# Kernel tuning notes

Measured on AMD Instinct MI355X. Metric: run time of the kernel, lower is better.

## Reference

```python
import jax, jax.numpy as jnp
import numpy as np

CLAMP = 5.0

def setup_inputs() -> dict:
    key = jax.random.key(0)
    k1, k2, k3, k4, k5 = jax.random.split(key, 5)
    B, S, D, R = 4, 4096, 2048, 16
    v = jax.random.normal(k1, (B, S, D), dtype=jnp.float32)
    x = jax.random.normal(k2, (B, S, D), dtype=jnp.float32)
    # params; match torch init scale (0.001) for U/W; V is zero-init in the module,
    # but use small random so the modulation branch is exercised.
    U = jax.random.normal(k3, (D, R), dtype=jnp.float32) * 0.001
    W = jax.random.normal(k4, (D, R), dtype=jnp.float32) * 0.001
    Vw = jax.random.normal(k5, (1, D), dtype=jnp.float32) * 0.01
    return {"v": v, "x": x, "U": U, "W": W, "Vw": Vw}

def reference(v, x, U, W, Vw):
    # proj: [B,S,R] ; sq elementwise ; out: [B,S,D]
    proj = jnp.einsum('bsd,dr->bsr', v, U)
    sq = proj * proj
    out = jnp.einsum('bsr,dr->bsd', sq, W)
    # dynamic curvature modulation: sigmoid(V^T x), V is Linear(dim,1,no bias)
    modulation = jax.nn.sigmoid(jnp.einsum('bsd,od->bso', x, Vw))  # [B,S,1]
    out = out * (1.0 + modulation)
    return jnp.clip(out, -CLAMP, CLAMP)
```

## Files before the change

### kernel.cpp

```cpp
#include <hip/hip_runtime.h>
#include <math.h>


constexpr int D_DIM   = 2048;
constexpr int R_DIM   = 16;
constexpr int ROWS    = 64;
constexpr int THREADS = 1024;
constexpr int WAVES   = THREADS / 64;
constexpr int RB      = 2;

typedef float f32x2 __attribute__((ext_vector_type(2)));

constexpr int SMEM_FLOATS = R_DIM * D_DIM + D_DIM + ROWS * R_DIM + ROWS;
constexpr size_t SMEM_BYTES = (size_t)SMEM_FLOATS * sizeof(float);

__device__ __forceinline__ float clamp5(float v) {
    return fminf(fmaxf(v, -5.0f), 5.0f);
}
__device__ __forceinline__ float dot4(float4 a, float4 b) {
    return a.x * b.x + a.y * b.y + a.z * b.z + a.w * b.w;
}

extern "C" __global__ void __launch_bounds__(THREADS)
__attribute__((amdgpu_waves_per_eu(4, 4)))
lrc_kernel(const float* __restrict__ v, const float* __restrict__ x,
           const float* __restrict__ U, const float* __restrict__ W,
           const float* __restrict__ Vw, float* __restrict__ out, int nrows)
{
    extern __shared__ float smem[];
    float* u_lds   = smem;
    float* vw_lds  = u_lds + R_DIM * D_DIM;
    float* sq_lds  = vw_lds + D_DIM;
    float* fac_lds = sq_lds + ROWS * R_DIM;

    const int tid  = threadIdx.x;
    const int lane = tid & 63;
    const int wave = tid >> 6;
    const int row0 = blockIdx.x * ROWS;

    for (int i = tid; i < D_DIM / 4; i += THREADS)
        reinterpret_cast<float4*>(vw_lds)[i] = reinterpret_cast<const float4*>(Vw)[i];

    {
        const int dd = tid * 2;
        float u0[R_DIM], u1[R_DIM];
        const float4* p0 = reinterpret_cast<const float4*>(U + (size_t)dd * R_DIM);
        const float4* p1 = reinterpret_cast<const float4*>(U + (size_t)(dd + 1) * R_DIM);
        #pragma unroll
        for (int c = 0; c < 4; ++c) {
            *reinterpret_cast<float4*>(&u0[c * 4]) = p0[c];
            *reinterpret_cast<float4*>(&u1[c * 4]) = p1[c];
        }
        #pragma unroll
        for (int r = 0; r < R_DIM; ++r)
            *reinterpret_cast<float2*>(&u_lds[r * D_DIM + dd]) = make_float2(u0[r], u1[r]);
    }
    __syncthreads();

    #pragma unroll
    for (int b = 0; b < (ROWS / WAVES) / RB; ++b) {
        const int rl0 = wave * (ROWS / WAVES) + b * RB;
        const float* vb = v + (size_t)(row0 + rl0) * D_DIM;
        const float* xb = x + (size_t)(row0 + rl0) * D_DIM;

        float pp[RB][R_DIM];
        float xv[RB];
        #pragma unroll
        for (int k = 0; k < RB; ++k) {
            xv[k] = 0.0f;
            #pragma unroll
            for (int r = 0; r < R_DIM; ++r) pp[k][r] = 0.0f;
        }

        for (int i = 0; i < D_DIM / 256; ++i) {
            const int d0 = i * 256 + lane * 4;
            float4 v4[RB], x4[RB];
            #pragma unroll
            for (int k = 0; k < RB; ++k) {
                v4[k] = *reinterpret_cast<const float4*>(vb + (size_t)k * D_DIM + d0);
                x4[k] = *reinterpret_cast<const float4*>(xb + (size_t)k * D_DIM + d0);
            }
            const float4 vw4 = *reinterpret_cast<const float4*>(vw_lds + d0);
            #pragma unroll
            for (int k = 0; k < RB; ++k) xv[k] += dot4(x4[k], vw4);
            #pragma unroll
            for (int r = 0; r < R_DIM; ++r) {
                const float4 u4 = *reinterpret_cast<const float4*>(u_lds + r * D_DIM + d0);
                #pragma unroll
                for (int k = 0; k < RB; ++k) pp[k][r] += dot4(v4[k], u4);
            }
        }

        #pragma unroll
        for (int s = 32; s >= 1; s >>= 1) {
            #pragma unroll
            for (int k = 0; k < RB; ++k) {
                xv[k] += __shfl_xor(xv[k], s, 64);
                #pragma unroll
                for (int r = 0; r < R_DIM; ++r) pp[k][r] += __shfl_xor(pp[k][r], s, 64);
            }
        }
        if (lane == 0) {
            #pragma unroll
            for (int k = 0; k < RB; ++k) {
                const int rl = rl0 + k;
                if (row0 + rl < nrows) {
                    #pragma unroll
                    for (int r = 0; r < R_DIM; ++r)
                        sq_lds[rl * R_DIM + r] = pp[k][r] * pp[k][r];
                    fac_lds[rl] = 1.0f + 1.0f / (1.0f + __expf(-xv[k]));
                }
            }
        }
    }
    __syncthreads();

    {
        const int dd = tid * 2;
        float w0[R_DIM], w1[R_DIM];
        const float4* p0 = reinterpret_cast<const float4*>(W + (size_t)dd * R_DIM);
        const float4* p1 = reinterpret_cast<const float4*>(W + (size_t)(dd + 1) * R_DIM);
        #pragma unroll
        for (int c = 0; c < 4; ++c) {
            *reinterpret_cast<float4*>(&w0[c * 4]) = p0[c];
            *reinterpret_cast<float4*>(&w1[c * 4]) = p1[c];
        }

        for (int rl = 0; rl < ROWS; ++rl) {
            if (row0 + rl >= nrows) break;
            float sqv[R_DIM];
            #pragma unroll
            for (int c = 0; c < 4; ++c)
                *reinterpret_cast<float4*>(&sqv[c * 4]) =
                    *reinterpret_cast<const float4*>(sq_lds + rl * R_DIM + c * 4);
            const float fac = fac_lds[rl];
            float o0 = 0.0f, o1 = 0.0f;
            #pragma unroll
            for (int r = 0; r < R_DIM; ++r) {
                o0 += sqv[r] * w0[r];
                o1 += sqv[r] * w1[r];
            }
            f32x2 o;
            o.x = clamp5(o0 * fac);
            o.y = clamp5(o1 * fac);
            __builtin_nontemporal_store(o,
                reinterpret_cast<f32x2*>(out + (size_t)(row0 + rl) * D_DIM + dd));
        }
    }
}

extern "C" void kernel_launch(void* const* d_in, const int* in_sizes, int n_in,
                              void* d_out, int out_size, void* d_ws, size_t ws_size,
                              hipStream_t stream) {
    const float* v  = (const float*)d_in[0];
    const float* x  = (const float*)d_in[1];
    const float* U  = (const float*)d_in[2];
    const float* W  = (const float*)d_in[3];
    const float* Vw = (const float*)d_in[4];
    float* out = (float*)d_out;

    const int nrows = in_sizes[0] / D_DIM;
    const int grid  = (nrows + ROWS - 1) / ROWS;

    (void)hipFuncSetAttribute((const void*)lrc_kernel,
                              hipFuncAttributeMaxDynamicSharedMemorySize,
                              (int)SMEM_BYTES);
    lrc_kernel<<<grid, THREADS, SMEM_BYTES, stream>>>(v, x, U, W, Vw, out, nrows);
}
```

Before: 84.52 us.

## Pre-transpose U in separate kernel, read U/Vw from global instead of LDS

Adds a small kernel that transposes U into the workspace so the main kernel can read U and Vw directly from global memory (through the caches) rather than staging them in 128 KB of LDS per block. Rows per block are halved to 32, so each wave handles a single pair of rows, and the forced waves-per-EU attribute is removed. The aim is to drop the per-block LDS fill and its sync and to let more blocks fit per CU. In exchange it adds an extra kernel launch and puts the per-iteration U reads on the cache hierarchy instead of LDS.

```diff
diff --git a/kernel.cpp b/kernel.cpp
--- a/kernel.cpp
+++ b/kernel.cpp
@@ -4,15 +4,12 @@
 
 constexpr int D_DIM   = 2048;
 constexpr int R_DIM   = 16;
-constexpr int ROWS    = 64;
+constexpr int ROWS    = 32;
 constexpr int THREADS = 1024;
 constexpr int WAVES   = THREADS / 64;
 constexpr int RB      = 2;
 
 typedef float f32x2 __attribute__((ext_vector_type(2)));
-
-constexpr int SMEM_FLOATS = R_DIM * D_DIM + D_DIM + ROWS * R_DIM + ROWS;
-constexpr size_t SMEM_BYTES = (size_t)SMEM_FLOATS * sizeof(float);
 
 __device__ __forceinline__ float clamp5(float v) {
     return fminf(fmaxf(v, -5.0f), 5.0f);
@@ -21,45 +18,31 @@
     return a.x * b.x + a.y * b.y + a.z * b.z + a.w * b.w;
 }
 
+extern "C" __global__ void transpose_u(const float* __restrict__ U,
+                                       float* __restrict__ Ut) {
+    const int o = blockIdx.x * blockDim.x + threadIdx.x;
+    if (o < R_DIM * D_DIM) {
+        const int r = o >> 11;
+        const int d = o & (D_DIM - 1);
+        Ut[o] = U[(d << 4) + r];
+    }
+}
+
 extern "C" __global__ void __launch_bounds__(THREADS)
-__attribute__((amdgpu_waves_per_eu(4, 4)))
 lrc_kernel(const float* __restrict__ v, const float* __restrict__ x,
-           const float* __restrict__ U, const float* __restrict__ W,
+           const float* __restrict__ Ut, const float* __restrict__ W,
            const float* __restrict__ Vw, float* __restrict__ out, int nrows)
 {
-    extern __shared__ float smem[];
-    float* u_lds   = smem;
-    float* vw_lds  = u_lds + R_DIM * D_DIM;
-    float* sq_lds  = vw_lds + D_DIM;
-    float* fac_lds = sq_lds + ROWS * R_DIM;
+    __shared__ float sq_lds[ROWS * R_DIM];
+    __shared__ float fac_lds[ROWS];
 
     const int tid  = threadIdx.x;
     const int lane = tid & 63;
     const int wave = tid >> 6;
     const int row0 = blockIdx.x * ROWS;
 
-    for (int i = tid; i < D_DIM / 4; i += THREADS)
-        reinterpret_cast<float4*>(vw_lds)[i] = reinterpret_cast<const float4*>(Vw)[i];
-
     {
-        const int dd = tid * 2;
-        float u0[R_DIM], u1[R_DIM];
-        const float4* p0 = reinterpret_cast<const float4*>(U + (size_t)dd * R_DIM);
-        const float4* p1 = reinterpret_cast<const float4*>(U + (size_t)(dd + 1) * R_DIM);
-        #pragma unroll
-        for (int c = 0; c < 4; ++c) {
-            *reinterpret_cast<float4*>(&u0[c * 4]) = p0[c];
-            *reinterpret_cast<float4*>(&u1[c * 4]) = p1[c];
-        }
-        #pragma unroll
-        for (int r = 0; r < R_DIM; ++r)
-            *reinterpret_cast<float2*>(&u_lds[r * D_DIM + dd]) = make_float2(u0[r], u1[r]);
-    }
-    __syncthreads();
-
-    #pragma unroll
-    for (int b = 0; b < (ROWS / WAVES) / RB; ++b) {
-        const int rl0 = wave * (ROWS / WAVES) + b * RB;
+        const int rl0 = wave * RB;
         const float* vb = v + (size_t)(row0 + rl0) * D_DIM;
         const float* xb = x + (size_t)(row0 + rl0) * D_DIM;
 
@@ -80,12 +63,13 @@
                 v4[k] = *reinterpret_cast<const float4*>(vb + (size_t)k * D_DIM + d0);
                 x4[k] = *reinterpret_cast<const float4*>(xb + (size_t)k * D_DIM + d0);
             }
-            const float4 vw4 = *reinterpret_cast<const float4*>(vw_lds + d0);
+            const float4 vw4 = *reinterpret_cast<const float4*>(Vw + d0);
             #pragma unroll
             for (int k = 0; k < RB; ++k) xv[k] += dot4(x4[k], vw4);
             #pragma unroll
             for (int r = 0; r < R_DIM; ++r) {
-                const float4 u4 = *reinterpret_cast<const float4*>(u_lds + r * D_DIM + d0);
+                const float4 u4 =
+                    *reinterpret_cast<const float4*>(Ut + r * D_DIM + d0);
                 #pragma unroll
                 for (int k = 0; k < RB; ++k) pp[k][r] += dot4(v4[k], u4);
             }
@@ -158,12 +142,11 @@
     const float* W  = (const float*)d_in[3];
     const float* Vw = (const float*)d_in[4];
     float* out = (float*)d_out;
+    float* Ut  = (float*)d_ws;
 
     const int nrows = in_sizes[0] / D_DIM;
     const int grid  = (nrows + ROWS - 1) / ROWS;
 
-    (void)hipFuncSetAttribute((const void*)lrc_kernel,
-                              hipFuncAttributeMaxDynamicSharedMemorySize,
-                              (int)SMEM_BYTES);
-    lrc_kernel<<<grid, THREADS, SMEM_BYTES, stream>>>(v, x, U, W, Vw, out, nrows);
+    transpose_u<<<(R_DIM * D_DIM + 255) / 256, 256, 0, stream>>>(U, Ut);
+    lrc_kernel<<<grid, THREADS, 0, stream>>>(v, x, Ut, W, Vw, out, nrows);
 }
```

Result: slower. 145.7 us (+72.4%).

## Keep per-row projections in registers and compute output per wave with transposed W

Applied to the files above, without the earlier changes.

Each wave now owns 4 rows end-to-end: it computes the rank-16 projections and modulation, squares them in registers, then directly produces the output rows using a pre-transposed W read as float4 from global memory. This removes the LDS staging of squared projections and the block-wide barrier between the reduction and output phases, and widens stores to float4. It adds a small extra transpose kernel launch per call, drops the partial-tail handling for incomplete row groups, and raises register pressure with RB=4 plus 16 float4 W values.

```diff
diff --git a/kernel.cpp b/kernel.cpp
--- a/kernel.cpp
+++ b/kernel.cpp
@@ -6,12 +6,11 @@
 constexpr int R_DIM   = 16;
 constexpr int ROWS    = 64;
 constexpr int THREADS = 1024;
-constexpr int WAVES   = THREADS / 64;
-constexpr int RB      = 2;
+constexpr int RB      = 4;
 
-typedef float f32x2 __attribute__((ext_vector_type(2)));
+typedef float f32x4 __attribute__((ext_vector_type(4)));
 
-constexpr int SMEM_FLOATS = R_DIM * D_DIM + D_DIM + ROWS * R_DIM + ROWS;
+constexpr int SMEM_FLOATS = R_DIM * D_DIM + D_DIM;
 constexpr size_t SMEM_BYTES = (size_t)SMEM_FLOATS * sizeof(float);
 
 __device__ __forceinline__ float clamp5(float v) {
@@ -21,17 +20,25 @@
     return a.x * b.x + a.y * b.y + a.z * b.z + a.w * b.w;
 }
 
+extern "C" __global__ void transpose_w(const float* __restrict__ W,
+                                       float* __restrict__ Wt) {
+    const int o = blockIdx.x * blockDim.x + threadIdx.x;
+    if (o < R_DIM * D_DIM) {
+        const int r = o >> 11;
+        const int d = o & (D_DIM - 1);
+        Wt[o] = W[(d << 4) + r];
+    }
+}
+
 extern "C" __global__ void __launch_bounds__(THREADS)
 __attribute__((amdgpu_waves_per_eu(4, 4)))
 lrc_kernel(const float* __restrict__ v, const float* __restrict__ x,
-           const float* __restrict__ U, const float* __restrict__ W,
+           const float* __restrict__ U, const float* __restrict__ Wt,
            const float* __restrict__ Vw, float* __restrict__ out, int nrows)
 {
     extern __shared__ float smem[];
-    float* u_lds   = smem;
-    float* vw_lds  = u_lds + R_DIM * D_DIM;
-    float* sq_lds  = vw_lds + D_DIM;
-    float* fac_lds = sq_lds + ROWS * R_DIM;
+    float* u_lds  = smem;
+    float* vw_lds = u_lds + R_DIM * D_DIM;
 
     const int tid  = threadIdx.x;
     const int lane = tid & 63;
@@ -57,94 +64,82 @@
     }
     __syncthreads();
 
+    const int rl0 = wave * RB;
+    const float* vb = v + (size_t)(row0 + rl0) * D_DIM;
+    const float* xb = x + (size_t)(row0 + rl0) * D_DIM;
+
+    float pp[RB][R_DIM];
+    float xv[RB];
     #pragma unroll
-    for (int b = 0; b < (ROWS / WAVES) / RB; ++b) {
-        const int rl0 = wave * (ROWS / WAVES) + b * RB;
-        const float* vb = v + (size_t)(row0 + rl0) * D_DIM;
-        const float* xb = x + (size_t)(row0 + rl0) * D_DIM;
+    for (int k = 0; k < RB; ++k) {
+        xv[k] = 0.0f;
+        #pragma unroll
+        for (int r = 0; r < R_DIM; ++r) pp[k][r] = 0.0f;
+    }
 
-        float pp[RB][R_DIM];
-        float xv[RB];
+    for (int i = 0; i < D_DIM / 256; ++i) {
+        const int d0 = i * 256 + lane * 4;
+        float4 v4[RB], x4[RB];
         #pragma unroll
         for (int k = 0; k < RB; ++k) {
-            xv[k] = 0.0f;
+            v4[k] = *reinterpret_cast<const float4*>(vb + (size_t)k * D_DIM + d0);
+            x4[k] = *reinterpret_cast<const float4*>(xb + (size_t)k * D_DIM + d0);
+        }
+        const float4 vw4 = *reinterpret_cast<const float4*>(vw_lds + d0);
+        #pragma unroll
+        for (int k = 0; k < RB; ++k) xv[k] += dot4(x4[k], vw4);
+        #pragma unroll
+        for (int r = 0; r < R_DIM; ++r) {
+            const float4 u4 = *reinterpret_cast<const float4*>(u_lds + r * D_DIM + d0);
             #pragma unroll
-            for (int r = 0; r < R_DIM; ++r) pp[k][r] = 0.0f;
+            for (int k = 0; k < RB; ++k) pp[k][r] += dot4(v4[k], u4);
         }
+    }
 
+    #pragma unroll
+    for (int s = 32; s >= 1; s >>= 1) {
+        #pragma unroll
+        for (int k = 0; k < RB; ++k) {
+            xv[k] += __shfl_xor(xv[k], s, 64);
+            #pragma unroll
+            for (int r = 0; r < R_DIM; ++r) pp[k][r] += __shfl_xor(pp[k][r], s, 64);
+        }
+    }
+
+    float fac[RB];
+    #pragma unroll
+    for (int k = 0; k < RB; ++k) {
+        fac[k] = 1.0f + 1.0f / (1.0f + __expf(-xv[k]));
+        #pragma unroll
+        for (int r = 0; r < R_DIM; ++r) pp[k][r] = pp[k][r] * pp[k][r];
+    }
+
+    if (row0 + rl0 + RB <= nrows) {
+        float* ob = out + (size_t)(row0 + rl0) * D_DIM;
         for (int i = 0; i < D_DIM / 256; ++i) {
             const int d0 = i * 256 + lane * 4;
-            float4 v4[RB], x4[RB];
+            float4 wt4[R_DIM];
+            #pragma unroll
+            for (int r = 0; r < R_DIM; ++r)
+                wt4[r] = *reinterpret_cast<const float4*>(Wt + r * D_DIM + d0);
             #pragma unroll
             for (int k = 0; k < RB; ++k) {
-                v4[k] = *reinterpret_cast<const float4*>(vb + (size_t)k * D_DIM + d0);
-                x4[k] = *reinterpret_cast<const float4*>(xb + (size_t)k * D_DIM + d0);
+                float4 o = make_float4(0.f, 0.f, 0.f, 0.f);
+                #pragma unroll
+                for (int r = 0; r < R_DIM; ++r) {
+                    o.x += pp[k][r] * wt4[r].x;
+                    o.y += pp[k][r] * wt4[r].y;
+                    o.z += pp[k][r] * wt4[r].z;
+                    o.w += pp[k][r] * wt4[r].w;
+                }
+                f32x4 ov;
+                ov.x = clamp5(o.x * fac[k]);
+                ov.y = clamp5(o.y * fac[k]);
+                ov.z = clamp5(o.z * fac[k]);
+                ov.w = clamp5(o.w * fac[k]);
+                __builtin_nontemporal_store(ov,
+                    reinterpret_cast<f32x4*>(ob + (size_t)k * D_DIM + d0));
             }
-            const float4 vw4 = *reinterpret_cast<const float4*>(vw_lds + d0);
-            #pragma unroll
-            for (int k = 0; k < RB; ++k) xv[k] += dot4(x4[k], vw4);
-            #pragma unroll
-            for (int r = 0; r < R_DIM; ++r) {
-                const float4 u4 = *reinterpret_cast<const float4*>(u_lds + r * D_DIM + d0);
-                #pragma unroll
-                for (int k = 0; k < RB; ++k) pp[k][r] += dot4(v4[k], u4);
-            }
-        }
-
-        #pragma unroll
-        for (int s = 32; s >= 1; s >>= 1) {
-            #pragma unroll
-            for (int k = 0; k < RB; ++k) {
-                xv[k] += __shfl_xor(xv[k], s, 64);
-                #pragma unroll
-                for (int r = 0; r < R_DIM; ++r) pp[k][r] += __shfl_xor(pp[k][r], s, 64);
-            }
-        }
-        if (lane == 0) {
-            #pragma unroll
-            for (int k = 0; k < RB; ++k) {
-                const int rl = rl0 + k;
-                if (row0 + rl < nrows) {
-                    #pragma unroll
-                    for (int r = 0; r < R_DIM; ++r)
-                        sq_lds[rl * R_DIM + r] = pp[k][r] * pp[k][r];
-                    fac_lds[rl] = 1.0f + 1.0f / (1.0f + __expf(-xv[k]));
-                }
-            }
-        }
-    }
-    __syncthreads();
-
-    {
-        const int dd = tid * 2;
-        float w0[R_DIM], w1[R_DIM];
-        const float4* p0 = reinterpret_cast<const float4*>(W + (size_t)dd * R_DIM);
-        const float4* p1 = reinterpret_cast<const float4*>(W + (size_t)(dd + 1) * R_DIM);
-        #pragma unroll
-        for (int c = 0; c < 4; ++c) {
-            *reinterpret_cast<float4*>(&w0[c * 4]) = p0[c];
-            *reinterpret_cast<float4*>(&w1[c * 4]) = p1[c];
-        }
-
-        for (int rl = 0; rl < ROWS; ++rl) {
-            if (row0 + rl >= nrows) break;
-            float sqv[R_DIM];
-            #pragma unroll
-            for (int c = 0; c < 4; ++c)
-                *reinterpret_cast<float4*>(&sqv[c * 4]) =
-                    *reinterpret_cast<const float4*>(sq_lds + rl * R_DIM + c * 4);
-            const float fac = fac_lds[rl];
-            float o0 = 0.0f, o1 = 0.0f;
-            #pragma unroll
-            for (int r = 0; r < R_DIM; ++r) {
-                o0 += sqv[r] * w0[r];
-                o1 += sqv[r] * w1[r];
-            }
-            f32x2 o;
-            o.x = clamp5(o0 * fac);
-            o.y = clamp5(o1 * fac);
-            __builtin_nontemporal_store(o,
-                reinterpret_cast<f32x2*>(out + (size_t)(row0 + rl) * D_DIM + dd));
         }
     }
 }
@@ -158,12 +153,15 @@
     const float* W  = (const float*)d_in[3];
     const float* Vw = (const float*)d_in[4];
     float* out = (float*)d_out;
+    float* Wt  = (float*)d_ws;
 
     const int nrows = in_sizes[0] / D_DIM;
     const int grid  = (nrows + ROWS - 1) / ROWS;
 
+    transpose_w<<<(R_DIM * D_DIM + 255) / 256, 256, 0, stream>>>(W, Wt);
+
     (void)hipFuncSetAttribute((const void*)lrc_kernel,
                               hipFuncAttributeMaxDynamicSharedMemorySize,
                               (int)SMEM_BYTES);
-    lrc_kernel<<<grid, THREADS, SMEM_BYTES, stream>>>(v, x, U, W, Vw, out, nrows);
+    lrc_kernel<<<grid, THREADS, SMEM_BYTES, stream>>>(v, x, U, Wt, Vw, out, nrows);
 }
```

After: 106.5 us. 26.1% more time.
